# Kernel tuning notes

Hardware: AMD Instinct MI355X
Metric: run time of the kernel (lower is better)

Reference implementation:

```python
import jax, jax.numpy as jnp
import numpy as np

HEIGHT = 108
WIDTH = 108
LEN_CLASSES = 7
EPS = 1e-5


def layout_bbox(pred, H, W):
    # pred: [B, O, 4 + LEN_CLASSES]
    bbox = pred[..., :4]
    cls_prob = pred[..., 4:]  # [B,O,7]
    x_c = bbox[..., 0] * W   # [B,O]
    y_c = bbox[..., 1] * H
    w = bbox[..., 2] * W
    h = bbox[..., 3] * H
    x1 = (x_c - 0.5 * w)[:, :, None, None]  # [B,O,1,1]
    x2 = (x_c + 0.5 * w)[:, :, None, None]
    y1 = (y_c - 0.5 * h)[:, :, None, None]
    y2 = (y_c + 0.5 * h)[:, :, None, None]
    xt = jnp.arange(W, dtype=pred.dtype)[None, None, None, :]  # [1,1,1,W]
    yt = jnp.arange(H, dtype=pred.dtype)[None, None, :, None]  # [1,1,H,1]
    x1d = xt - x1  # [B,O,1,W]
    x2d = x2 - xt
    y1d = yt - y1  # [B,O,H,1]
    y2d = y2 - yt
    # min(relu(d), 1) == clip(d, 0, 1)
    yband = jnp.clip(y1d, 0.0, 1.0) * jnp.clip(y2d, 0.0, 1.0)  # [B,O,H,1]
    xband = jnp.clip(x1d, 0.0, 1.0) * jnp.clip(x2d, 0.0, 1.0)  # [B,O,1,W]
    x1_line = jax.nn.relu(1.0 - jnp.abs(x1d)) * yband  # [B,O,H,W]
    x2_line = jax.nn.relu(1.0 - jnp.abs(x2d)) * yband
    y1_line = jax.nn.relu(1.0 - jnp.abs(y1d)) * xband
    y2_line = jax.nn.relu(1.0 - jnp.abs(y2d)) * xband
    xy_max = jnp.maximum(jnp.maximum(x1_line, x2_line), jnp.maximum(y1_line, y2_line))  # [B,O,H,W]
    spatial = xy_max[..., None] * cls_prob[:, :, None, None, :]  # [B,O,H,W,7]
    return jnp.max(spatial, axis=1)  # [B,H,W,7]


def bn(x, g, b, axes):
    m = jnp.mean(x, axis=axes, keepdims=True)
    v = jnp.var(x, axis=axes, keepdims=True)
    shape = [1] * x.ndim
    shape[1 if x.ndim == 4 else -1] = -1
    return (x - m) * jax.lax.rsqrt(v + EPS) * g.reshape(shape) + b.reshape(shape)


def conv2d(x, w, b, stride):
    y = jax.lax.conv_general_dilated(x, w, (stride, stride), 'VALID',
                                     dimension_numbers=('NCHW', 'OIHW', 'NCHW'))
    return y + b[None, :, None, None]


def setup_inputs() -> dict:
    key = jax.random.key(0)
    ks = jax.random.split(key, 16)
    B, O = 64, 16
    d = {}
    d['image'] = jax.random.uniform(ks[0], (B, O, 4 + LEN_CLASSES), dtype=jnp.float32)
    d['conv1_w'] = jax.random.normal(ks[1], (32, LEN_CLASSES, 5, 5), jnp.float32) * 0.05
    d['conv1_b'] = jnp.zeros((32,), jnp.float32)
    d['bn1_g'] = jnp.ones((32,), jnp.float32)
    d['bn1_b'] = jnp.zeros((32,), jnp.float32)
    d['conv2_w'] = jax.random.normal(ks[2], (64, 32, 5, 5), jnp.float32) * 0.03
    d['conv2_b'] = jnp.zeros((64,), jnp.float32)
    d['bn2_g'] = jnp.ones((64,), jnp.float32)
    d['bn2_b'] = jnp.zeros((64,), jnp.float32)
    d['fc1_w'] = jax.random.normal(ks[3], (512, 36864), jnp.float32) * 0.005
    d['fc1_b'] = jnp.zeros((512,), jnp.float32)
    d['bn3_g'] = jnp.ones((512,), jnp.float32)
    d['bn3_b'] = jnp.zeros((512,), jnp.float32)
    d['fc2_w'] = jax.random.normal(ks[4], (1, 512), jnp.float32) * 0.04
    d['fc2_b'] = jnp.zeros((1,), jnp.float32)
    return d


def reference(image, conv1_w, conv1_b, bn1_g, bn1_b, conv2_w, conv2_b, bn2_g, bn2_b,
              fc1_w, fc1_b, bn3_g, bn3_b, fc2_w, fc2_b):
    # layout_bbox(image, WIDTH, HEIGHT): output_height=WIDTH, output_width=HEIGHT (both 108)
    layout = layout_bbox(image, WIDTH, HEIGHT)           # [B,108,108,7]
    x = jnp.transpose(layout, (0, 3, 1, 2))              # [B,7,108,108]
    x = conv2d(x, conv1_w, conv1_b, 2)                   # [B,32,52,52]
    x = bn(x, bn1_g, bn1_b, (0, 2, 3))
    x = jax.nn.leaky_relu(x, 0.2)
    x = conv2d(x, conv2_w, conv2_b, 2)                   # [B,64,24,24]
    x = bn(x, bn2_g, bn2_b, (0, 2, 3))
    x = jax.nn.leaky_relu(x, 0.2)
    x = x.reshape(x.shape[0], -1)                        # [B,36864]
    x = x @ fc1_w.T + fc1_b                              # [B,512]
    x = bn(x, bn3_g, bn3_b, (0,))
    x = jax.nn.leaky_relu(x, 0.2)
    x = x @ fc2_w.T + fc2_b                              # [B,1]
    return jax.nn.sigmoid(x)
```

## Files before the change

### kernel.cpp

```cpp
#include <hip/hip_runtime.h>
#include <hip/hip_bf16.h>


typedef unsigned short u16;
typedef __attribute__((ext_vector_type(8))) short bf8_t;
typedef __attribute__((ext_vector_type(4))) float f4_t;
#define MFMA16(a, b, c) __builtin_amdgcn_mfma_f32_16x16x32_bf16(a, b, c, 0, 0, 0)

#define LEAKY(v) (fmaxf((v), 0.2f * (v)))
#define CLIP01(v) fminf(fmaxf((v), 0.0f), 1.0f)

__device__ inline unsigned f2bf(float f) {
  unsigned u = __float_as_uint(f);
  return (u + 0x7FFFu + ((u >> 16) & 1u)) >> 16;
}
__device__ inline float bf2f(unsigned u) { return __uint_as_float(u << 16); }

constexpr int HW = 108;
constexpr int NOBJ = 16;
constexpr int NCLS = 7;

__global__ __launch_bounds__(128) void layout_prep_kernel(
    const float* __restrict__ image, const float* __restrict__ w1,
    const float* __restrict__ w2, u16* __restrict__ lay8,
    u16* __restrict__ wB1, u16* __restrict__ wB2, float* __restrict__ st) {
  int h = blockIdx.x, b = blockIdx.y;
  int tid = threadIdx.x;
  int bid = b * 108 + h;
  if (bid < 114) {
#pragma unroll
    for (int j = 0; j < 4; ++j) {
      int i = bid * 512 + j * 128 + tid;
      if (i < 1216) st[i] = 0.f;
      if (i < 7168) {
        int co = i / 224, k = i % 224;
        int chunk = k >> 5, kk = k & 31, tl = kk >> 3, ci = kk & 7;
        int tap = chunk * 4 + tl;
        unsigned v = 0;
        if (tap < 25 && ci < 7) v = f2bf(w1[co * 175 + ci * 25 + tap]);
        wB1[i] = (u16)v;
      } else if (i < 58368) {
        int jj = i - 7168;
        int tap = jj / 2048, r = jj % 2048, co = r >> 5, ci = r & 31;
        wB2[jj] = (u16)f2bf(w2[co * 800 + ci * 25 + tap]);
      }
    }
  }
  __shared__ float sIm[NOBJ * 11];
  for (int i = tid; i < NOBJ * 11; i += 128) sIm[i] = image[b * NOBJ * 11 + i];
  __syncthreads();
  int w = tid;
  if (w >= HW) return;
  float best[NCLS];
#pragma unroll
  for (int c = 0; c < NCLS; ++c) best[c] = 0.0f;
  float fw = (float)w, fh = (float)h;
  for (int o = 0; o < NOBJ; ++o) {
    const float* p = &sIm[o * 11];
    float xc = p[0] * 108.0f, yc = p[1] * 108.0f;
    float wd = p[2] * 108.0f, hd = p[3] * 108.0f;
    float x1 = xc - 0.5f * wd, x2 = xc + 0.5f * wd;
    float y1 = yc - 0.5f * hd, y2 = yc + 0.5f * hd;
    float x1d = fw - x1, x2d = x2 - fw;
    float y1d = fh - y1, y2d = y2 - fh;
    float yband = CLIP01(y1d) * CLIP01(y2d);
    float xband = CLIP01(x1d) * CLIP01(x2d);
    float x1l = fmaxf(1.0f - fabsf(x1d), 0.0f) * yband;
    float x2l = fmaxf(1.0f - fabsf(x2d), 0.0f) * yband;
    float y1l = fmaxf(1.0f - fabsf(y1d), 0.0f) * xband;
    float y2l = fmaxf(1.0f - fabsf(y2d), 0.0f) * xband;
    float xy = fmaxf(fmaxf(x1l, x2l), fmaxf(y1l, y2l));
#pragma unroll
    for (int c = 0; c < NCLS; ++c) best[c] = fmaxf(best[c], xy * p[4 + c]);
  }
  unsigned p0 = f2bf(best[0]) | (f2bf(best[1]) << 16);
  unsigned p1 = f2bf(best[2]) | (f2bf(best[3]) << 16);
  unsigned p2 = f2bf(best[4]) | (f2bf(best[5]) << 16);
  unsigned p3 = f2bf(best[6]);
  uint4 stv = {p0, p1, p2, p3};
  ((uint4*)lay8)[b * 11664 + h * 108 + w] = stv;
}

__global__ __launch_bounds__(128) void conv1_mfma(
    const u16* __restrict__ lay8, const u16* __restrict__ wB1,
    u16* __restrict__ x1r, float* __restrict__ bn1sum,
    float* __restrict__ bn1sq) {
  int mtg = blockIdx.x, nt = blockIdx.y, bz = blockIdx.z;
  int tid = threadIdx.x;
  int lane = tid & 63, wv = tid >> 6;
  int f = lane & 15, q = lane >> 4;
  int co = nt * 16 + f;
  int b0 = bz * 4 + wv * 2;
  int pbase[4];
  bool mvalid[4];
#pragma unroll
  for (int t = 0; t < 4; ++t) {
    int mt = mtg * 4 + t;
    mvalid[t] = mt < 169;
    int P = min(mt * 16 + f, 2703);
    int oh = P / 52, ow = P - oh * 52;
    pbase[t] = (oh * 2 * 108 + ow * 2) * 8;
  }
  f4_t acc[2][4];
#pragma unroll
  for (int b2 = 0; b2 < 2; ++b2)
#pragma unroll
    for (int t = 0; t < 4; ++t) acc[b2][t] = {0.f, 0.f, 0.f, 0.f};
#pragma unroll
  for (int chunk = 0; chunk < 7; ++chunk) {
    int tap = chunk * 4 + q;
    tap = tap > 24 ? 24 : tap;
    int kh = tap / 5, kw = tap - kh * 5;
    int toff = (kh * 108 + kw) * 8;
    bf8_t bf = *(const bf8_t*)&wB1[co * 224 + chunk * 32 + q * 8];
#pragma unroll
    for (int b2 = 0; b2 < 2; ++b2) {
      const u16* lb = lay8 + (size_t)(b0 + b2) * 93312;
#pragma unroll
      for (int t = 0; t < 4; ++t) {
        bf8_t af = *(const bf8_t*)&lb[pbase[t] + toff];
        acc[b2][t] = MFMA16(af, bf, acc[b2][t]);
      }
    }
  }
  float s = 0.f, sq = 0.f;
#pragma unroll
  for (int b2 = 0; b2 < 2; ++b2) {
    u16* ob = x1r + (size_t)(b0 + b2) * 86528;
#pragma unroll
    for (int t = 0; t < 4; ++t) {
      if (!mvalid[t]) continue;
      int P0 = (mtg * 4 + t) * 16 + q * 4;
#pragma unroll
      for (int r = 0; r < 4; ++r) {
        float v = acc[b2][t][r];
        s += v;
        sq += v * v;
        ob[(P0 + r) * 32 + co] = (u16)f2bf(v);
      }
    }
  }
  s += __shfl_xor(s, 16);
  s += __shfl_xor(s, 32);
  sq += __shfl_xor(sq, 16);
  sq += __shfl_xor(sq, 32);
  __shared__ float rs[2][16], rq[2][16];
  if (lane < 16) {
    rs[wv][f] = s;
    rq[wv][f] = sq;
  }
  __syncthreads();
  if (tid < 16) {
    atomicAdd(&bn1sum[nt * 16 + tid], rs[0][tid] + rs[1][tid]);
    atomicAdd(&bn1sq[nt * 16 + tid], rq[0][tid] + rq[1][tid]);
  }
}

__global__ __launch_bounds__(256) void bnapply1_kernel(
    const u16* __restrict__ x1r, const float* __restrict__ bn1sum,
    const float* __restrict__ bn1sq, const float* __restrict__ g1,
    const float* __restrict__ b1, u16* __restrict__ x1b) {
  int idx = blockIdx.x * 256 + threadIdx.x;
  int base = idx * 8, c0 = base & 31;
  float sc[8], sh[8];
#pragma unroll
  for (int j = 0; j < 8; ++j) {
    int c = c0 + j;
    float mean = bn1sum[c] * (1.f / 173056.f);
    float var = bn1sq[c] * (1.f / 173056.f) - mean * mean;
    float s = g1[c] * rsqrtf(var + 1e-5f);
    sc[j] = s;
    sh[j] = b1[c] - mean * s;
  }
  uint4 in = *(const uint4*)&x1r[base];
  unsigned w[4] = {in.x, in.y, in.z, in.w};
  unsigned out[4];
#pragma unroll
  for (int j = 0; j < 4; ++j) {
    float a = bf2f(w[j] & 0xffffu);
    float bq = bf2f(w[j] >> 16);
    a = LEAKY(fmaf(a, sc[2 * j], sh[2 * j]));
    bq = LEAKY(fmaf(bq, sc[2 * j + 1], sh[2 * j + 1]));
    out[j] = f2bf(a) | (f2bf(bq) << 16);
  }
  uint4 stv = {out[0], out[1], out[2], out[3]};
  *(uint4*)&x1b[base] = stv;
}

__global__ __launch_bounds__(256) void conv2_mfma(
    const u16* __restrict__ x1b, const u16* __restrict__ wB2,
    u16* __restrict__ x2b, float* __restrict__ bn2sum,
    float* __restrict__ bn2sq) {
  int mt = blockIdx.x, ntg = blockIdx.y, bz = blockIdx.z;
  int tid = threadIdx.x;
  int lane = tid & 63, wv = tid >> 6;
  int f = lane & 15, q = lane >> 4;
  int co0 = ntg * 32;
  int b0 = bz * 16 + wv * 4;
  int P = mt * 16 + f;
  int oh = P / 24, ow = P - oh * 24;
  int abase = (oh * 2 * 52 + ow * 2) * 32 + q * 8;
  f4_t acc[4][2];
#pragma unroll
  for (int b2 = 0; b2 < 4; ++b2)
#pragma unroll
    for (int n = 0; n < 2; ++n) acc[b2][n] = {0.f, 0.f, 0.f, 0.f};
#pragma unroll
  for (int tap = 0; tap < 25; ++tap) {
    int kh = tap / 5, kw = tap - kh * 5;
    int toff = (kh * 52 + kw) * 32;
    bf8_t bf0 = *(const bf8_t*)&wB2[tap * 2048 + (co0 + f) * 32 + q * 8];
    bf8_t bf1 = *(const bf8_t*)&wB2[tap * 2048 + (co0 + 16 + f) * 32 + q * 8];
#pragma unroll
    for (int b2 = 0; b2 < 4; ++b2) {
      bf8_t af =
          *(const bf8_t*)&x1b[(size_t)(b0 + b2) * 86528 + abase + toff];
      acc[b2][0] = MFMA16(af, bf0, acc[b2][0]);
      acc[b2][1] = MFMA16(af, bf1, acc[b2][1]);
    }
  }
  float s[2] = {0.f, 0.f}, sq[2] = {0.f, 0.f};
#pragma unroll
  for (int b2 = 0; b2 < 4; ++b2) {
    u16* ob = x2b + (size_t)(b0 + b2) * 36864;
#pragma unroll
    for (int n = 0; n < 2; ++n)
#pragma unroll
      for (int r = 0; r < 4; ++r) {
        float v = acc[b2][n][r];
        s[n] += v;
        sq[n] += v * v;
        ob[(mt * 16 + q * 4 + r) * 64 + co0 + n * 16 + f] = (u16)f2bf(v);
      }
  }
#pragma unroll
  for (int n = 0; n < 2; ++n) {
    s[n] += __shfl_xor(s[n], 16);
    s[n] += __shfl_xor(s[n], 32);
    sq[n] += __shfl_xor(sq[n], 16);
    sq[n] += __shfl_xor(sq[n], 32);
  }
  __shared__ float rs[4][32], rq[4][32];
  if (lane < 16) {
#pragma unroll
    for (int n = 0; n < 2; ++n) {
      rs[wv][n * 16 + f] = s[n];
      rq[wv][n * 16 + f] = sq[n];
    }
  }
  __syncthreads();
  if (tid < 32) {
    atomicAdd(&bn2sum[co0 + tid],
              rs[0][tid] + rs[1][tid] + rs[2][tid] + rs[3][tid]);
    atomicAdd(&bn2sq[co0 + tid],
              rq[0][tid] + rq[1][tid] + rq[2][tid] + rq[3][tid]);
  }
}

__global__ __launch_bounds__(256) void bnapply2t_kernel(
    const u16* __restrict__ x2b, const float* __restrict__ bn2sum,
    const float* __restrict__ bn2sq, const float* __restrict__ g2,
    const float* __restrict__ b2, u16* __restrict__ xB) {
  int hw0 = blockIdx.x * 64, b = blockIdx.y;
  __shared__ float tile[64 * 65];
  int t = threadIdx.x;
  int c = t & 63, hl4 = t >> 6;
  float mean = bn2sum[c] * (1.f / 36864.f);
  float var = bn2sq[c] * (1.f / 36864.f) - mean * mean;
  float s = g2[c] * rsqrtf(var + 1e-5f);
  float h = b2[c] - mean * s;
#pragma unroll
  for (int it = 0; it < 16; ++it) {
    int hl = it * 4 + hl4;
    float v = bf2f((unsigned)x2b[((size_t)b * 576 + hw0 + hl) * 64 + c]);
    tile[hl * 65 + c] = LEAKY(fmaf(v, s, h));
  }
  __syncthreads();
  int hw = t & 63, cl4 = t >> 6;
#pragma unroll
  for (int it = 0; it < 16; ++it) {
    int cc = it * 4 + cl4;
    xB[(size_t)b * 36864 + cc * 576 + hw0 + hw] = (u16)f2bf(tile[hw * 65 + cc]);
  }
}

__global__ __launch_bounds__(256, 4) void fc1_mfma(
    const u16* __restrict__ xB, const float* __restrict__ wgt,
    float* __restrict__ part) {
  int ks = blockIdx.x, nb = blockIdx.y;
  int tid = threadIdx.x;
  int lane = tid & 63, wv = tid >> 6;
  int f = lane & 15, q = lane >> 4;
  int n0 = nb * 64 + wv * 16;
  int kbase = ks * 512;
  f4_t acc[4];
#pragma unroll
  for (int m = 0; m < 4; ++m) acc[m] = {0.f, 0.f, 0.f, 0.f};
  const float* wrow = wgt + (size_t)(n0 + f) * 36864 + kbase + q * 8;
  const u16* arow = xB + (size_t)f * 36864 + kbase + q * 8;
#pragma unroll 4
  for (int kt = 0; kt < 16; ++kt) {
    const float* wp = wrow + kt * 32;
    float4 wa = *(const float4*)wp;
    float4 wb = *(const float4*)(wp + 4);
    bf8_t afr[4];
#pragma unroll
    for (int m = 0; m < 4; ++m)
      afr[m] = *(const bf8_t*)&arow[(size_t)m * 589824 + kt * 32];
    union { bf8_t v; u16 u[8]; } bu;
    bu.u[0] = (u16)f2bf(wa.x); bu.u[1] = (u16)f2bf(wa.y);
    bu.u[2] = (u16)f2bf(wa.z); bu.u[3] = (u16)f2bf(wa.w);
    bu.u[4] = (u16)f2bf(wb.x); bu.u[5] = (u16)f2bf(wb.y);
    bu.u[6] = (u16)f2bf(wb.z); bu.u[7] = (u16)f2bf(wb.w);
#pragma unroll
    for (int m = 0; m < 4; ++m) acc[m] = MFMA16(afr[m], bu.v, acc[m]);
  }
  float* pp = part + (size_t)ks * 32768;
#pragma unroll
  for (int m = 0; m < 4; ++m)
#pragma unroll
    for (int r = 0; r < 4; ++r)
      pp[(m * 16 + q * 4 + r) * 512 + n0 + f] = acc[m][r];
}

__global__ __launch_bounds__(256) void fc1_reduce_kernel(
    const float* __restrict__ part, float* __restrict__ fc1o,
    float* __restrict__ bn3sum, float* __restrict__ bn3sq) {
  int i = blockIdx.x * 256 + threadIdx.x;
  float s = 0.f;
#pragma unroll 8
  for (int ks = 0; ks < 72; ++ks) s += part[(size_t)ks * 32768 + i];
  fc1o[i] = s;
  atomicAdd(&bn3sum[i & 511], s);
  atomicAdd(&bn3sq[i & 511], s * s);
}

__global__ __launch_bounds__(64) void fc2_kernel(
    const float* __restrict__ fc1o, const float* __restrict__ bn3sum,
    const float* __restrict__ bn3sq, const float* __restrict__ g3,
    const float* __restrict__ b3, const float* __restrict__ w2,
    const float* __restrict__ b2o, float* __restrict__ out) {
  int m = blockIdx.x;
  int fl = threadIdx.x;
  float a = 0.f;
#pragma unroll
  for (int j = 0; j < 8; ++j) {
    int ff = fl + j * 64;
    float mean = bn3sum[ff] * (1.f / 64.f);
    float var = bn3sq[ff] * (1.f / 64.f) - mean * mean;
    float sc = g3[ff] * rsqrtf(var + 1e-5f);
    float sh = b3[ff] - mean * sc;
    float v = LEAKY(fmaf(fc1o[m * 512 + ff], sc, sh));
    a += v * w2[ff];
  }
  for (int off = 32; off; off >>= 1) a += __shfl_down(a, off, 64);
  if (fl == 0) out[m] = 1.f / (1.f + expf(-(a + b2o[0])));
}

extern "C" void kernel_launch(void* const* d_in, const int* in_sizes, int n_in,
                              void* d_out, int out_size, void* d_ws,
                              size_t ws_size, hipStream_t stream) {
  const float* image = (const float*)d_in[0];
  const float* c1w = (const float*)d_in[1];
  const float* bn1g = (const float*)d_in[3];
  const float* bn1b = (const float*)d_in[4];
  const float* c2w = (const float*)d_in[5];
  const float* bn2g = (const float*)d_in[7];
  const float* bn2b = (const float*)d_in[8];
  const float* f1w = (const float*)d_in[9];
  const float* bn3g = (const float*)d_in[11];
  const float* bn3b = (const float*)d_in[12];
  const float* f2w = (const float*)d_in[13];
  const float* f2b = (const float*)d_in[14];
  float* ws = (float*)d_ws;

  u16* lay8 = (u16*)ws;
  u16* x1r = (u16*)(ws + 2985984);
  u16* x1b = (u16*)(ws + 5754880);
  u16* x2b = (u16*)(ws + 8523776);
  u16* xB = (u16*)(ws + 9703424);
  float* fc1part = ws + 10883072;
  float* fc1o = ws + 13242368;
  float* st = ws + 13275136;
  float* bn1sum = st, *bn1sq = st + 32;
  float* bn2sum = st + 64, *bn2sq = st + 128;
  float* bn3sum = st + 192, *bn3sq = st + 704;
  u16* wB1 = (u16*)(ws + 13276352);
  u16* wB2 = (u16*)(ws + 13279936);

  layout_prep_kernel<<<dim3(108, 64), 128, 0, stream>>>(image, c1w, c2w, lay8,
                                                        wB1, wB2, st);
  conv1_mfma<<<dim3(43, 2, 16), 128, 0, stream>>>(lay8, wB1, x1r, bn1sum,
                                                  bn1sq);
  bnapply1_kernel<<<2704, 256, 0, stream>>>(x1r, bn1sum, bn1sq, bn1g, bn1b,
                                            x1b);
  conv2_mfma<<<dim3(36, 2, 4), 256, 0, stream>>>(x1b, wB2, x2b, bn2sum,
                                                 bn2sq);
  bnapply2t_kernel<<<dim3(9, 64), 256, 0, stream>>>(x2b, bn2sum, bn2sq, bn2g,
                                                    bn2b, xB);
  fc1_mfma<<<dim3(72, 8), 256, 0, stream>>>(xB, f1w, fc1part);
  fc1_reduce_kernel<<<128, 256, 0, stream>>>(fc1part, fc1o, bn3sum, bn3sq);
  fc2_kernel<<<64, 64, 0, stream>>>(fc1o, bn3sum, bn3sq, bn3g, bn3b, f2w, f2b,
                                    (float*)d_out);
}
```

Baseline: 251.4 us.

## Replace fc1 split-K partial buffer and reduce kernel with atomic accumulation

The fc1 split-K GEMM now adds its partial tiles straight into the zero-initialised fc1 output with float atomics, using twice as many K slices. This removes the 72-slice partial buffer write, the separate reduce kernel launch and its re-read of that buffer. BN3 statistics are now computed inside fc2, with each block recomputing the per-feature mean and variance over all 64 rows. The cost is 144-way atomic contention per output element, nondeterministic summation order, and redundant statistics work in every fc2 block.

Result: slower. 259.8 us (+3.3%).

```diff
diff --git a/kernel.cpp b/kernel.cpp
--- a/kernel.cpp
+++ b/kernel.cpp
@@ -23,7 +23,8 @@
 __global__ __launch_bounds__(128) void layout_prep_kernel(
     const float* __restrict__ image, const float* __restrict__ w1,
     const float* __restrict__ w2, u16* __restrict__ lay8,
-    u16* __restrict__ wB1, u16* __restrict__ wB2, float* __restrict__ st) {
+    u16* __restrict__ wB1, u16* __restrict__ wB2, float* __restrict__ st,
+    float* __restrict__ fc1o) {
   int h = blockIdx.x, b = blockIdx.y;
   int tid = threadIdx.x;
   int bid = b * 108 + h;
@@ -45,6 +46,10 @@
         wB2[jj] = (u16)f2bf(w2[co * 800 + ci * 25 + tap]);
       }
     }
+  } else if (bid < 178) {
+    int zb = bid - 114;
+#pragma unroll
+    for (int j = 0; j < 4; ++j) fc1o[zb * 512 + j * 128 + tid] = 0.f;
   }
   __shared__ float sIm[NOBJ * 11];
   for (int i = tid; i < NOBJ * 11; i += 128) sIm[i] = image[b * NOBJ * 11 + i];
@@ -286,20 +291,20 @@
 
 __global__ __launch_bounds__(256, 4) void fc1_mfma(
     const u16* __restrict__ xB, const float* __restrict__ wgt,
-    float* __restrict__ part) {
+    float* __restrict__ fc1o) {
   int ks = blockIdx.x, nb = blockIdx.y;
   int tid = threadIdx.x;
   int lane = tid & 63, wv = tid >> 6;
   int f = lane & 15, q = lane >> 4;
   int n0 = nb * 64 + wv * 16;
-  int kbase = ks * 512;
+  int kbase = ks * 256;
   f4_t acc[4];
 #pragma unroll
   for (int m = 0; m < 4; ++m) acc[m] = {0.f, 0.f, 0.f, 0.f};
   const float* wrow = wgt + (size_t)(n0 + f) * 36864 + kbase + q * 8;
   const u16* arow = xB + (size_t)f * 36864 + kbase + q * 8;
 #pragma unroll 4
-  for (int kt = 0; kt < 16; ++kt) {
+  for (int kt = 0; kt < 8; ++kt) {
     const float* wp = wrow + kt * 32;
     float4 wa = *(const float4*)wp;
     float4 wb = *(const float4*)(wp + 4);
@@ -315,46 +320,53 @@
 #pragma unroll
     for (int m = 0; m < 4; ++m) acc[m] = MFMA16(afr[m], bu.v, acc[m]);
   }
-  float* pp = part + (size_t)ks * 32768;
 #pragma unroll
   for (int m = 0; m < 4; ++m)
 #pragma unroll
     for (int r = 0; r < 4; ++r)
-      pp[(m * 16 + q * 4 + r) * 512 + n0 + f] = acc[m][r];
-}
-
-__global__ __launch_bounds__(256) void fc1_reduce_kernel(
-    const float* __restrict__ part, float* __restrict__ fc1o,
-    float* __restrict__ bn3sum, float* __restrict__ bn3sq) {
-  int i = blockIdx.x * 256 + threadIdx.x;
-  float s = 0.f;
-#pragma unroll 8
-  for (int ks = 0; ks < 72; ++ks) s += part[(size_t)ks * 32768 + i];
-  fc1o[i] = s;
-  atomicAdd(&bn3sum[i & 511], s);
-  atomicAdd(&bn3sq[i & 511], s * s);
-}
-
-__global__ __launch_bounds__(64) void fc2_kernel(
-    const float* __restrict__ fc1o, const float* __restrict__ bn3sum,
-    const float* __restrict__ bn3sq, const float* __restrict__ g3,
+      atomicAdd(&fc1o[(m * 16 + q * 4 + r) * 512 + n0 + f], acc[m][r]);
+}
+
+__global__ __launch_bounds__(256) void fc2_kernel(
+    const float* __restrict__ fc1o, const float* __restrict__ g3,
     const float* __restrict__ b3, const float* __restrict__ w2,
     const float* __restrict__ b2o, float* __restrict__ out) {
   int m = blockIdx.x;
-  int fl = threadIdx.x;
+  int t = threadIdx.x;
+  __shared__ float ssc[512], ssh[512];
+  __shared__ float red[4];
+#pragma unroll
+  for (int jj = 0; jj < 2; ++jj) {
+    int ff = t + jj * 256;
+    float s = 0.f, sq = 0.f;
+#pragma unroll 8
+    for (int mm = 0; mm < 64; ++mm) {
+      float v = fc1o[mm * 512 + ff];
+      s += v;
+      sq += v * v;
+    }
+    float mean = s * (1.f / 64.f);
+    float var = sq * (1.f / 64.f) - mean * mean;
+    float sc = g3[ff] * rsqrtf(var + 1e-5f);
+    ssc[ff] = sc;
+    ssh[ff] = b3[ff] - mean * sc;
+  }
+  __syncthreads();
   float a = 0.f;
 #pragma unroll
-  for (int j = 0; j < 8; ++j) {
-    int ff = fl + j * 64;
-    float mean = bn3sum[ff] * (1.f / 64.f);
-    float var = bn3sq[ff] * (1.f / 64.f) - mean * mean;
-    float sc = g3[ff] * rsqrtf(var + 1e-5f);
-    float sh = b3[ff] - mean * sc;
-    float v = LEAKY(fmaf(fc1o[m * 512 + ff], sc, sh));
+  for (int jj = 0; jj < 2; ++jj) {
+    int ff = t + jj * 256;
+    float v = LEAKY(fmaf(fc1o[m * 512 + ff], ssc[ff], ssh[ff]));
     a += v * w2[ff];
   }
   for (int off = 32; off; off >>= 1) a += __shfl_down(a, off, 64);
-  if (fl == 0) out[m] = 1.f / (1.f + expf(-(a + b2o[0])));
+  int lane = t & 63, wv = t >> 6;
+  if (lane == 0) red[wv] = a;
+  __syncthreads();
+  if (t == 0) {
+    float tot = red[0] + red[1] + red[2] + red[3];
+    out[m] = 1.f / (1.f + expf(-(tot + b2o[0])));
+  }
 }
 
 extern "C" void kernel_launch(void* const* d_in, const int* in_sizes, int n_in,
@@ -379,17 +391,15 @@
   u16* x1b = (u16*)(ws + 5754880);
   u16* x2b = (u16*)(ws + 8523776);
   u16* xB = (u16*)(ws + 9703424);
-  float* fc1part = ws + 10883072;
-  float* fc1o = ws + 13242368;
-  float* st = ws + 13275136;
+  float* fc1o = ws + 10883072;
+  float* st = ws + 10915840;
   float* bn1sum = st, *bn1sq = st + 32;
   float* bn2sum = st + 64, *bn2sq = st + 128;
-  float* bn3sum = st + 192, *bn3sq = st + 704;
-  u16* wB1 = (u16*)(ws + 13276352);
-  u16* wB2 = (u16*)(ws + 13279936);
+  u16* wB1 = (u16*)(ws + 10917056);
+  u16* wB2 = (u16*)(ws + 10920640);
 
   layout_prep_kernel<<<dim3(108, 64), 128, 0, stream>>>(image, c1w, c2w, lay8,
-                                                        wB1, wB2, st);
+                                                        wB1, wB2, st, fc1o);
   conv1_mfma<<<dim3(43, 2, 16), 128, 0, stream>>>(lay8, wB1, x1r, bn1sum,
                                                   bn1sq);
   bnapply1_kernel<<<2704, 256, 0, stream>>>(x1r, bn1sum, bn1sq, bn1g, bn1b,
@@ -398,8 +408,7 @@
                                                  bn2sq);
   bnapply2t_kernel<<<dim3(9, 64), 256, 0, stream>>>(x2b, bn2sum, bn2sq, bn2g,
                                                     bn2b, xB);
-  fc1_mfma<<<dim3(72, 8), 256, 0, stream>>>(xB, f1w, fc1part);
-  fc1_reduce_kernel<<<128, 256, 0, stream>>>(fc1part, fc1o, bn3sum, bn3sq);
-  fc2_kernel<<<64, 64, 0, stream>>>(fc1o, bn3sum, bn3sq, bn3g, bn3b, f2w, f2b,
-                                    (float*)d_out);
-}
+  fc1_mfma<<<dim3(144, 8), 256, 0, stream>>>(xB, f1w, fc1o);
+  fc2_kernel<<<64, 256, 0, stream>>>(fc1o, bn3g, bn3b, f2w, f2b,
+                                     (float*)d_out);
+}
```
